# Kernel tuning notes

Hardware: AMD Instinct MI355X
Metric: run time of the kernel (lower is better)

## Reference

```python
import jax, jax.numpy as jnp
import numpy as np

# dims
T, B, D = 128, 512, 512          # seq, batch, d_input = dim_aug_state*n_agent
M, H, DH, DFF = 6, 2, 32, 64     # mem_len, heads, d_head_inner, d_ff_inner
ACT = 64                          # dim_action*n_agent
BG = 0.1                          # GRU-gate bias (GTrXL)


def _ln(t, g, b):
    mu = t.mean(-1, keepdims=True)
    var = ((t - mu) ** 2).mean(-1, keepdims=True)
    return (t - mu) / jnp.sqrt(var + 1e-5) * g + b


def _rel_shift(x):
    # x: [T, J, B, H] -> TransformerXL relative shift
    Tq, J = x.shape[0], x.shape[1]
    zp = jnp.zeros((Tq, 1) + x.shape[2:], x.dtype)
    x = jnp.concatenate([zp, x], axis=1)              # [T, J+1, B, H]
    x = x.reshape((J + 1, Tq) + x.shape[2:])[1:]      # [J, T, B, H]
    return x.reshape((Tq, J) + x.shape[2:])


def _gate(x, y, W, b):
    # GRU-style gating g(x, y): x = residual stream, y = new branch output
    lin = lambda t, i: t @ W[i] + b[i]
    r = jax.nn.sigmoid(lin(y, 0) + lin(x, 1))
    z = jax.nn.sigmoid(lin(y, 2) + lin(x, 3) - BG)
    h = jnp.tanh(lin(y, 4) + (r * x) @ W[5] + b[5])
    return (1.0 - z) * x + z * h


def setup_inputs() -> dict:
    key = jax.random.key(0)
    ks = iter(jax.random.split(key, 32))
    rn = lambda shape, s=0.02: jax.random.normal(next(ks), shape, jnp.float32) * s
    return dict(
        aug_states=jax.random.normal(next(ks), (T, B, D), jnp.float32),
        action=jax.random.normal(next(ks), (B, ACT), jnp.float32),
        memory=jnp.zeros((M, B, D), jnp.float32),
        W_q=rn((D, H * DH)), W_kv=rn((D, 2 * H * DH)), W_p=rn((D, H * DH)), W_out=rn((H * DH, D)),
        u=rn((H, DH)), v=rn((H, DH)),
        ln1_g=jnp.ones(D), ln1_b=jnp.zeros(D), ln2_g=jnp.ones(D), ln2_b=jnp.zeros(D),
        ff_W1=rn((D, DFF)), ff_b1=jnp.zeros(DFF), ff_W2=rn((DFF, D)), ff_b2=jnp.zeros(D),
        g1_W=rn((6, D, D)), g1_b=jnp.zeros((6, D)), g2_W=rn((6, D, D)), g2_b=jnp.zeros((6, D)),
        d1_W=rn((D, 1024)), d1_b=jnp.zeros(1024),
        d2_W=rn((1024 + ACT, 512)), d2_b=jnp.zeros(512),
        d3_W=rn((512, 300)), d3_b=jnp.zeros(300),
        d4_W=rn((300, 1)), d4_b=jnp.zeros(1),
    )


def reference(aug_states, action, memory, W_q, W_kv, W_p, W_out, u, v,
              ln1_g, ln1_b, ln2_g, ln2_b, ff_W1, ff_b1, ff_W2, ff_b2,
              g1_W, g1_b, g2_W, g2_b, d1_W, d1_b, d2_W, d2_b, d3_W, d3_b, d4_W, d4_b):
    x = aug_states                                    # [T, B, D]
    J = T + M
    # sinusoidal relative position embeddings for positions J-1 .. 0
    pos = jnp.arange(J - 1, -1, -1.0, dtype=jnp.float32)
    inv_freq = 1.0 / (10000.0 ** (jnp.arange(0, D, 2, dtype=jnp.float32) / D))
    si = pos[:, None] * inv_freq[None, :]
    pos_emb = jnp.concatenate([jnp.sin(si), jnp.cos(si)], axis=-1)   # [J, D]

    # --- stable (pre-LN + gated) TransformerXL layer ---
    src2 = _ln(x, ln1_g, ln1_b)
    cat = jnp.concatenate([memory, src2], axis=0)     # [J, B, D]
    k, vv = jnp.split(cat @ W_kv, 2, axis=-1)
    q = (src2 @ W_q).reshape(T, B, H, DH)
    k = k.reshape(J, B, H, DH)
    vv = vv.reshape(J, B, H, DH)
    p = (pos_emb @ W_p).reshape(J, H, DH)
    content = jnp.einsum("ibhd,jbhd->ijbh", q + u, k)
    position = _rel_shift(jnp.einsum("ibhd,jhd->ijbh", q + v, p))
    attn = content + position                         # [T, J, B, H]
    mask = jnp.arange(J)[None, :] > (jnp.arange(T)[:, None] + M)     # causal w/ memory offset
    attn = jnp.where(mask[:, :, None, None], -jnp.inf, attn)
    attn = jax.nn.softmax(attn * (1.0 / np.sqrt(DH)), axis=1)
    av = jnp.einsum("ijbh,jbhd->ibhd", attn, vv).reshape(T, B, H * DH)
    src = _gate(x, av @ W_out, g1_W, g1_b)
    ff = jax.nn.relu(_ln(src, ln2_g, ln2_b) @ ff_W1 + ff_b1) @ ff_W2 + ff_b2
    out = _gate(src, ff, g2_W, g2_b)                  # [T, B, D]

    # --- mean pool + MLP critic head ---
    ts = out.mean(axis=0)                             # [B, D]
    h1 = jax.nn.relu(ts @ d1_W + d1_b)
    h = jnp.concatenate([h1, action], axis=1)
    h = jax.nn.relu(h @ d2_W + d2_b)
    h = jax.nn.relu(h @ d3_W + d3_b)
    return jax.nn.relu(h @ d4_W + d4_b)               # [B, 1]
```

## Files before the change

### kernel.cpp

```cpp
#include <hip/hip_runtime.h>
#include <math.h>

namespace {

constexpr int kT = 128, kB = 512, kD = 512, kM = 6, kH = 2;
constexpr int kJ = kT + kM;
constexpr float kBG = 0.1f;
constexpr int kTB = kT * kB;
constexpr int kBK = 32;

typedef __attribute__((ext_vector_type(8))) short bf16x8;
typedef __attribute__((ext_vector_type(4))) float f32x4;
typedef __attribute__((ext_vector_type(8))) unsigned short us8;
typedef __attribute__((ext_vector_type(4))) unsigned short us4;

__device__ __forceinline__ float sigmoidf_(float x) {
  return 1.0f / (1.0f + __expf(-x));
}

__device__ __forceinline__ unsigned short bf16u(float f) {
  union { float f; unsigned u; } c; c.f = f;
  unsigned r = c.u + 0x7fffu + ((c.u >> 16) & 1u);
  return (unsigned short)(r >> 16);
}

__device__ __forceinline__ float b2f(unsigned short u) {
  union { unsigned u; float f; } c; c.u = (unsigned)u << 16;
  return c.f;
}

__device__ __forceinline__ void gl_lds16(const void* g, void* l) {
  __builtin_amdgcn_global_load_lds(
      (const __attribute__((address_space(1))) unsigned int*)g,
      (__attribute__((address_space(3))) unsigned int*)l, 16, 0, 0);
}

template <int N>
__device__ __forceinline__ void wvm_() {
  asm volatile("s_waitcnt vmcnt(%0)" :: "n"(N) : "memory");
}
__device__ __forceinline__ void bar_() { __builtin_amdgcn_s_barrier(); }
__device__ __forceinline__ void cfence_() { asm volatile("" ::: "memory"); }


__global__ __launch_bounds__(256) void transp_kernel(const float* __restrict__ W,
                                                     unsigned short* __restrict__ Wt,
                                                     int K, int N) {
  __shared__ float t[32][33];
  const int n0 = blockIdx.x * 32, k0 = blockIdx.y * 32;
  const float* Wb = W + (size_t)blockIdx.z * K * N;
  unsigned short* Wtb = Wt + (size_t)blockIdx.z * K * N;
  int tx = threadIdx.x & 31, ty = threadIdx.x >> 5;
#pragma unroll
  for (int r = 0; r < 32; r += 8)
    t[ty + r][tx] = Wb[(size_t)(k0 + ty + r) * N + n0 + tx];
  __syncthreads();
#pragma unroll
  for (int r = 0; r < 32; r += 8)
    Wtb[(size_t)(n0 + ty + r) * K + k0 + tx] = bf16u(t[tx][ty + r]);
}

__global__ __launch_bounds__(256) void conv_bf16_kernel(const float* __restrict__ in,
                                                        unsigned short* __restrict__ outb,
                                                        size_t n) {
  size_t idx = ((size_t)blockIdx.x * 256 + threadIdx.x) * 8;
  if (idx >= n) return;
  float4 a = *(const float4*)(in + idx);
  float4 c = *(const float4*)(in + idx + 4);
  us8 o;
  o[0] = bf16u(a.x); o[1] = bf16u(a.y); o[2] = bf16u(a.z); o[3] = bf16u(a.w);
  o[4] = bf16u(c.x); o[5] = bf16u(c.y); o[6] = bf16u(c.z); o[7] = bf16u(c.w);
  *(us8*)(outb + idx) = o;
}

__global__ __launch_bounds__(256) void ln1_dual_kernel(const float* __restrict__ in,
                                                       const float* __restrict__ g,
                                                       const float* __restrict__ b,
                                                       unsigned short* __restrict__ outLN,
                                                       unsigned short* __restrict__ outRaw,
                                                       int nrows) {
  int wave = threadIdx.x >> 6, lane = threadIdx.x & 63;
  int row = blockIdx.x * 4 + wave;
  if (row >= nrows) return;
  const float* p = in + (size_t)row * kD + lane * 8;
  float4 a = *(const float4*)p;
  float4 c = *(const float4*)(p + 4);
  float v[8] = {a.x, a.y, a.z, a.w, c.x, c.y, c.z, c.w};
  float s = 0.f;
#pragma unroll
  for (int i = 0; i < 8; ++i) s += v[i];
#pragma unroll
  for (int off = 32; off; off >>= 1) s += __shfl_xor(s, off);
  float mu = s * (1.0f / 512.0f);
  float q = 0.f;
#pragma unroll
  for (int i = 0; i < 8; ++i) { float d = v[i] - mu; q += d * d; }
#pragma unroll
  for (int off = 32; off; off >>= 1) q += __shfl_xor(q, off);
  float rstd = rsqrtf(q * (1.0f / 512.0f) + 1e-5f);
  us8 oln, oraw;
#pragma unroll
  for (int i = 0; i < 8; ++i) {
    int col = lane * 8 + i;
    oln[i] = bf16u((v[i] - mu) * rstd * g[col] + b[col]);
    oraw[i] = bf16u(v[i]);
  }
  size_t off8 = (size_t)row * kD + lane * 8;
  *(us8*)(outLN + off8) = oln;
  *(us8*)(outRaw + off8) = oraw;
}

__global__ __launch_bounds__(256) void ln_b16_kernel(const unsigned short* __restrict__ in,
                                                     const float* __restrict__ g,
                                                     const float* __restrict__ b,
                                                     unsigned short* __restrict__ outb,
                                                     int nrows) {
  int wave = threadIdx.x >> 6, lane = threadIdx.x & 63;
  int row = blockIdx.x * 4 + wave;
  if (row >= nrows) return;
  us8 iv = *(const us8*)(in + (size_t)row * kD + lane * 8);
  float v[8];
#pragma unroll
  for (int i = 0; i < 8; ++i) v[i] = b2f(iv[i]);
  float s = 0.f;
#pragma unroll
  for (int i = 0; i < 8; ++i) s += v[i];
#pragma unroll
  for (int off = 32; off; off >>= 1) s += __shfl_xor(s, off);
  float mu = s * (1.0f / 512.0f);
  float q = 0.f;
#pragma unroll
  for (int i = 0; i < 8; ++i) { float d = v[i] - mu; q += d * d; }
#pragma unroll
  for (int off = 32; off; off >>= 1) q += __shfl_xor(q, off);
  float rstd = rsqrtf(q * (1.0f / 512.0f) + 1e-5f);
  us8 o;
#pragma unroll
  for (int i = 0; i < 8; ++i) {
    int col = lane * 8 + i;
    o[i] = bf16u((v[i] - mu) * rstd * g[col] + b[col]);
  }
  *(us8*)(outb + (size_t)row * kD + lane * 8) = o;
}

template <int TN, int EPI>
__global__ __launch_bounds__(256) void mfma_gemm_bt(
    const unsigned short* __restrict__ A, const unsigned short* __restrict__ Bt,
    int K, const float* __restrict__ bias, void* __restrict__ Cv, int N) {
  constexpr int MI = (TN == 128) ? 4 : 2;
  constexpr int NJ = 4;
  constexpr int BCH = TN * 64 / 1024;
  constexpr int NLD = 2 + BCH / 4;
  __shared__ __align__(16) unsigned short As[3][128 * kBK];
  __shared__ __align__(16) unsigned short Bs[3][TN * kBK];
  const int tid = threadIdx.x;
  const int lane = tid & 63, wv = tid >> 6;
  const int ml = lane & 15, qd = lane >> 4;
  const int swc = ((lane & 3) ^ ((lane >> 3) & 3)) * 16;
  const int qdx = qd ^ ((ml >> 1) & 3);
  const int m0 = blockIdx.y * 128, n0 = blockIdx.x * TN;
  const int mw0 = (TN == 128) ? (wv >> 1) * 64 : wv * 32;
  const int nw0 = (TN == 128) ? (wv & 1) * 64 : 0;
  const size_t ldA = (size_t)K * 2, ldB = (size_t)K * 2;
  const char* Ab = (const char*)A + (size_t)m0 * ldA;
  const char* Bb = (const char*)Bt + (size_t)n0 * ldB;
  auto stg = [&](int k0, int buf) {
#pragma unroll
    for (int c = wv; c < 8; c += 4) {
      int fb = c * 1024 + lane * 16;
      gl_lds16(Ab + (size_t)(fb >> 6) * ldA + swc + (size_t)k0 * 2,
               (char*)As[buf] + c * 1024 + lane * 16);
    }
#pragma unroll
    for (int c = wv; c < BCH; c += 4) {
      int fb = c * 1024 + lane * 16;
      gl_lds16(Bb + (size_t)(fb >> 6) * ldB + swc + (size_t)k0 * 2,
               (char*)Bs[buf] + c * 1024 + lane * 16);
    }
  };
  f32x4 acc[MI][NJ];
#pragma unroll
  for (int i = 0; i < MI; ++i)
#pragma unroll
    for (int j = 0; j < NJ; ++j) acc[i][j] = (f32x4)0.f;
  stg(0, 0);
  stg(kBK, 1);
  int cb = 0;
  for (int k0 = 0; k0 < K; k0 += kBK) {
    const int sb = (cb == 0) ? 2 : cb - 1;
    if (k0 + 2 * kBK < K) { stg(k0 + 2 * kBK, sb); wvm_<2 * NLD>(); }
    else if (k0 + kBK < K) { wvm_<NLD>(); }
    else { wvm_<0>(); }
    bar_(); cfence_();
    bf16x8 af[MI], bfr[NJ];
#pragma unroll
    for (int i = 0; i < MI; ++i)
      af[i] = *(const bf16x8*)(As[cb] + (mw0 + i * 16 + ml) * kBK + qdx * 8);
#pragma unroll
    for (int j = 0; j < NJ; ++j)
      bfr[j] = *(const bf16x8*)(Bs[cb] + (nw0 + j * 16 + ml) * kBK + qdx * 8);
#pragma unroll
    for (int i = 0; i < MI; ++i)
#pragma unroll
      for (int j = 0; j < NJ; ++j)
        acc[i][j] = __builtin_amdgcn_mfma_f32_16x16x32_bf16(af[i], bfr[j], acc[i][j], 0, 0, 0);
    cfence_(); bar_();
    cb = (cb == 2) ? 0 : cb + 1;
  }
#pragma unroll
  for (int i = 0; i < MI; ++i)
#pragma unroll
    for (int j = 0; j < NJ; ++j)
#pragma unroll
      for (int r = 0; r < 4; ++r) {
        int m = m0 + mw0 + i * 16 + qd * 4 + r;
        int n = n0 + nw0 + j * 16 + ml;
        float val = acc[i][j][r];
        if (EPI >= 2) val += bias[n];
        if (EPI == 2) val = fmaxf(val, 0.f);
        size_t idx = (size_t)m * N + n;
        if (EPI == 0) ((float*)Cv)[idx] = val;
        else ((unsigned short*)Cv)[idx] = bf16u(val);
      }
}

template <int NBLOG>
__device__ __forceinline__ void xcd_decode(int& m0, int& n0, int tileN) {
  const int L = blockIdx.x;
  const int xcd = L & 7;
  const int s = L >> 3;
  const int mgPerX = (int)(gridDim.x >> (3 + NBLOG));
  const int mg = xcd * mgPerX + (s >> NBLOG);
  const int nb = s & ((1 << NBLOG) - 1);
  m0 = mg * 128;
  n0 = nb * tileN;
}

__global__ __launch_bounds__(512, 4) void mfma_gate_rz(
    const unsigned short* __restrict__ Yb, const unsigned short* __restrict__ Xb,
    const unsigned short* __restrict__ Wt, const float* __restrict__ gb,
    unsigned short* __restrict__ RX, unsigned short* __restrict__ Zq) {
  __shared__ __align__(16) unsigned short As[3][128 * kBK];
  __shared__ __align__(16) unsigned short Bs[3][256 * kBK];
  const int tid = threadIdx.x;
  const int lane = tid & 63, wv = tid >> 6;
  const int ml = lane & 15, qd = lane >> 4;
  const int swc = ((lane & 3) ^ ((lane >> 3) & 3)) * 16;
  const int qdx = qd ^ ((ml >> 1) & 3);
  int m0, n0;
  xcd_decode<2>(m0, n0, 256);
  const int nhalf = n0 >> 9;
  const int n0e = n0 & 511;
  const int mw0 = (wv & 1) * 64, nw0 = (wv >> 1) * 64;
  const size_t ld = (size_t)kD * 2;
  const size_t DD = (size_t)kD * kD;
  const char* Abp[2], *Bbp[2];
  {
    const unsigned short* Ap[2] = {Yb, Xb};
#pragma unroll
    for (int p = 0; p < 2; ++p) {
      Abp[p] = (const char*)Ap[p] + (size_t)m0 * ld;
      Bbp[p] = (const char*)(Wt + (size_t)(2 * nhalf + p) * DD) + (size_t)n0e * ld;
    }
  }
  auto stg = [&](const char* Ab, const char* Bb, int k0, int buf) {
    {
      int fb = wv * 1024 + lane * 16;
      gl_lds16(Ab + (size_t)(fb >> 6) * ld + swc + (size_t)k0 * 2,
               (char*)As[buf] + fb);
    }
#pragma unroll
    for (int c = wv; c < 16; c += 8) {
      int fb = c * 1024 + lane * 16;
      gl_lds16(Bb + (size_t)(fb >> 6) * ld + swc + (size_t)k0 * 2,
               (char*)Bs[buf] + fb);
    }
  };
  f32x4 acc[4][4];
#pragma unroll
  for (int i = 0; i < 4; ++i)
#pragma unroll
    for (int j = 0; j < 4; ++j) acc[i][j] = (f32x4)0.f;
  stg(Abp[0], Bbp[0], 0, 0);
  stg(Abp[0], Bbp[0], kBK, 1);
  int cb = 0;
#pragma unroll
  for (int p = 0; p < 2; ++p) {
    for (int k = 0; k < 16; ++k) {
      const int sb = (cb == 0) ? 2 : cb - 1;
      if (k < 14) { stg(Abp[p], Bbp[p], (k + 2) * kBK, sb); wvm_<6>(); }
      else if (p < 1) { stg(Abp[p + 1], Bbp[p + 1], (k - 14) * kBK, sb); wvm_<6>(); }
      else if (k == 14) { wvm_<3>(); }
      else { wvm_<0>(); }
      bar_(); cfence_();
      bf16x8 af[4], bfr[4];
#pragma unroll
      for (int i = 0; i < 4; ++i)
        af[i] = *(const bf16x8*)(As[cb] + (mw0 + i * 16 + ml) * kBK + qdx * 8);
#pragma unroll
      for (int j = 0; j < 4; ++j)
        bfr[j] = *(const bf16x8*)(Bs[cb] + (nw0 + j * 16 + ml) * kBK + qdx * 8);
#pragma unroll
      for (int i = 0; i < 4; ++i)
#pragma unroll
        for (int j = 0; j < 4; ++j)
          acc[i][j] = __builtin_amdgcn_mfma_f32_16x16x32_bf16(af[i], bfr[j], acc[i][j], 0, 0, 0);
      cfence_(); bar_();
      cb = (cb == 2) ? 0 : cb + 1;
    }
  }
  if (nhalf == 0) {
#pragma unroll
    for (int i = 0; i < 4; ++i)
#pragma unroll
      for (int j = 0; j < 4; ++j)
#pragma unroll
        for (int r = 0; r < 4; ++r) {
          int m = m0 + mw0 + i * 16 + qd * 4 + r;
          int n = n0e + nw0 + j * 16 + ml;
          float rg = sigmoidf_(acc[i][j][r] + gb[n] + gb[kD + n]);
          size_t idx = (size_t)m * kD + n;
          RX[idx] = bf16u(rg * b2f(Xb[idx]));
        }
  } else {
#pragma unroll
    for (int i = 0; i < 4; ++i)
#pragma unroll
      for (int j = 0; j < 4; ++j)
#pragma unroll
        for (int r = 0; r < 4; ++r) {
          int m = m0 + mw0 + i * 16 + qd * 4 + r;
          int n = n0e + nw0 + j * 16 + ml;
          float z = sigmoidf_(acc[i][j][r] + gb[2 * kD + n] + gb[3 * kD + n] - kBG);
          Zq[(size_t)m * kD + n] = (unsigned short)(z * 65535.f + 0.5f);
        }
  }
}

template <bool POOL>
__global__ __launch_bounds__(512, 4) void mfma_gate_h(
    const unsigned short* __restrict__ Yb, const unsigned short* __restrict__ RXb,
    const unsigned short* __restrict__ Xb, const unsigned short* __restrict__ Wt,
    const float* __restrict__ gb, const unsigned short* __restrict__ Zq,
    unsigned short* __restrict__ OUTb, float* __restrict__ TS, int rowoff) {
  __shared__ __align__(16) unsigned short As[3][128 * kBK];
  __shared__ __align__(16) unsigned short Bs[3][256 * kBK];
  const int tid = threadIdx.x;
  const int lane = tid & 63, wv = tid >> 6;
  const int ml = lane & 15, qd = lane >> 4;
  const int swc = ((lane & 3) ^ ((lane >> 3) & 3)) * 16;
  const int qdx = qd ^ ((ml >> 1) & 3);
  int m0, n0;
  xcd_decode<1>(m0, n0, 256);
  const int mw0 = (wv & 1) * 64, nw0 = (wv >> 1) * 64;
  const size_t ld = (size_t)kD * 2;
  const size_t DD = (size_t)kD * kD;
  const char* Abp[2], *Bbp[2];
  {
    const unsigned short* Ap[2] = {Yb, RXb};
#pragma unroll
    for (int p = 0; p < 2; ++p) {
      Abp[p] = (const char*)Ap[p] + (size_t)m0 * ld;
      Bbp[p] = (const char*)(Wt + (size_t)(4 + p) * DD) + (size_t)n0 * ld;
    }
  }
  auto stg = [&](const char* Ab, const char* Bb, int k0, int buf) {
    {
      int fb = wv * 1024 + lane * 16;
      gl_lds16(Ab + (size_t)(fb >> 6) * ld + swc + (size_t)k0 * 2,
               (char*)As[buf] + fb);
    }
#pragma unroll
    for (int c = wv; c < 16; c += 8) {
      int fb = c * 1024 + lane * 16;
      gl_lds16(Bb + (size_t)(fb >> 6) * ld + swc + (size_t)k0 * 2,
               (char*)Bs[buf] + fb);
    }
  };
  f32x4 acc[4][4];
#pragma unroll
  for (int i = 0; i < 4; ++i)
#pragma unroll
    for (int j = 0; j < 4; ++j) acc[i][j] = (f32x4)0.f;
  stg(Abp[0], Bbp[0], 0, 0);
  stg(Abp[0], Bbp[0], kBK, 1);
  int cb = 0;
#pragma unroll
  for (int p = 0; p < 2; ++p) {
    for (int k = 0; k < 16; ++k) {
      const int sb = (cb == 0) ? 2 : cb - 1;
      if (k < 14) { stg(Abp[p], Bbp[p], (k + 2) * kBK, sb); wvm_<6>(); }
      else if (p < 1) { stg(Abp[p + 1], Bbp[p + 1], (k - 14) * kBK, sb); wvm_<6>(); }
      else if (k == 14) { wvm_<3>(); }
      else { wvm_<0>(); }
      bar_(); cfence_();
      bf16x8 af[4], bfr[4];
#pragma unroll
      for (int i = 0; i < 4; ++i)
        af[i] = *(const bf16x8*)(As[cb] + (mw0 + i * 16 + ml) * kBK + qdx * 8);
#pragma unroll
      for (int j = 0; j < 4; ++j)
        bfr[j] = *(const bf16x8*)(Bs[cb] + (nw0 + j * 16 + ml) * kBK + qdx * 8);
#pragma unroll
      for (int i = 0; i < 4; ++i)
#pragma unroll
        for (int j = 0; j < 4; ++j)
          acc[i][j] = __builtin_amdgcn_mfma_f32_16x16x32_bf16(af[i], bfr[j], acc[i][j], 0, 0, 0);
      cfence_(); bar_();
      cb = (cb == 2) ? 0 : cb + 1;
    }
  }
#pragma unroll
  for (int i = 0; i < 4; ++i)
#pragma unroll
    for (int j = 0; j < 4; ++j)
#pragma unroll
      for (int r = 0; r < 4; ++r) {
        int m = m0 + mw0 + i * 16 + qd * 4 + r;
        int n = n0 + nw0 + j * 16 + ml;
        size_t idx = (size_t)m * kD + n;
        float z = (float)Zq[idx] * (1.0f / 65535.0f);
        float hc = tanhf(acc[i][j][r] + gb[4 * kD + n] + gb[5 * kD + n]);
        float val = (1.0f - z) * b2f(Xb[idx]) + z * hc;
        if (POOL) {
          int b = (rowoff + m) & (kB - 1);
          atomicAdd(TS + (size_t)b * kD + n, val * (1.0f / kT));
        } else {
          OUTb[idx] = bf16u(val);
        }
      }
}

__global__ __launch_bounds__(64) void posp_kernel(const float* __restrict__ Wp,
                                                  float* __restrict__ P) {
  __shared__ float emb[512];
  int jj = blockIdx.x;
  int t = threadIdx.x;
  float pos = (float)(kJ - 1 - jj);
#pragma unroll
  for (int r = 0; r < 8; ++r) {
    int d = t + r * 64;
    int i = (d < 256) ? d : d - 256;
    float invf = expf(-((float)(2 * i) * (1.0f / 512.0f)) * 9.210340371976184f);
    float si = pos * invf;
    emb[d] = (d < 256) ? sinf(si) : cosf(si);
  }
  __syncthreads();
  float acc = 0.f;
  for (int d = 0; d < 512; ++d) acc = fmaf(emb[d], Wp[d * 64 + t], acc);
  P[jj * 64 + t] = acc;
}

__global__ __launch_bounds__(128) void attn_kernel(
    const float* __restrict__ Q, const unsigned short* __restrict__ KV,
    const float* __restrict__ P, const float* __restrict__ U,
    const float* __restrict__ V, unsigned short* __restrict__ AV) {
  __shared__ float ks[kJ][32];
  __shared__ float vs[kJ][32];
  __shared__ float ps[32][kJ + 2];
  const int b = blockIdx.x, h = blockIdx.y;
  const int tid = threadIdx.x;
  for (int idx = tid; idx < kJ * 8; idx += 128) {
    int j = idx >> 3, seg = idx & 7;
    const unsigned short* src = KV + ((size_t)(j * kB + b)) * 128 + h * 32 + seg * 4;
    us4 kq = *(const us4*)src;
    us4 vq = *(const us4*)(src + 64);
#pragma unroll
    for (int e = 0; e < 4; ++e) {
      ks[j][seg * 4 + e] = b2f(kq[e]);
      vs[j][seg * 4 + e] = b2f(vq[e]);
    }
  }
  for (int idx = tid; idx < kJ * 8; idx += 128) {
    int j = idx >> 3, seg = idx & 7;
    float4 pq = *(const float4*)(P + j * 64 + h * 32 + seg * 4);
    ps[seg * 4 + 0][j] = pq.x;
    ps[seg * 4 + 1][j] = pq.y;
    ps[seg * 4 + 2][j] = pq.z;
    ps[seg * 4 + 3][j] = pq.w;
  }
  __syncthreads();
  const int i = tid;
  float qu[32], qv[32];
  const float* qp = Q + ((size_t)(i * kB + b)) * 64 + h * 32;
#pragma unroll
  for (int d = 0; d < 32; ++d) {
    float qd = qp[d];
    qu[d] = qd + U[h * 32 + d];
    qv[d] = qd + V[h * 32 + d];
  }
  float m = -INFINITY, l = 0.f, acc[32] = {};
  const float scale = 0.17677669529663687f;
  for (int j = 0; j <= i + kM; ++j) {
    float s = 0.f;
#pragma unroll
    for (int d = 0; d < 32; d += 4) {
      float4 k4 = *(const float4*)&ks[j][d];
      s = fmaf(qu[d + 0], k4.x, s);
      s = fmaf(qu[d + 1], k4.y, s);
      s = fmaf(qu[d + 2], k4.z, s);
      s = fmaf(qu[d + 3], k4.w, s);
    }
    int jj = j + (kT - 1) - i;
#pragma unroll
    for (int d = 0; d < 32; ++d) s = fmaf(qv[d], ps[d][jj], s);
    float ls = s * scale;
    float nm = fmaxf(m, ls);
    float w = __expf(ls - nm);
    float f = __expf(m - nm);
    l = l * f + w;
#pragma unroll
    for (int d = 0; d < 32; d += 4) {
      float4 v4 = *(const float4*)&vs[j][d];
      acc[d + 0] = fmaf(acc[d + 0], f, w * v4.x);
      acc[d + 1] = fmaf(acc[d + 1], f, w * v4.y);
      acc[d + 2] = fmaf(acc[d + 2], f, w * v4.z);
      acc[d + 3] = fmaf(acc[d + 3], f, w * v4.w);
    }
    m = nm;
  }
  float inv = 1.0f / l;
  unsigned short* o = AV + ((size_t)(i * kB + b)) * 64 + h * 32;
#pragma unroll
  for (int d = 0; d < 32; ++d) o[d] = bf16u(acc[d] * inv);
}

template <int ACTF, bool DUAL>
__global__ __launch_bounds__(256) void gemm_kernel(
    const float* __restrict__ A1, const float* __restrict__ Bm1, int K1,
    const float* __restrict__ A2, const float* __restrict__ Bm2, int K2,
    const float* __restrict__ bias, float* __restrict__ C, int Mrows, int N) {
  __shared__ float As[16][68];
  __shared__ float Bs[16][68];
  const int tid = threadIdx.x;
  const int tx = tid & 15, ty = tid >> 4;
  const int m0 = blockIdx.y * 64, n0 = blockIdx.x * 64;
  const int ar = tid >> 2, aseg = tid & 3;
  float acc[4][4] = {};
#pragma unroll
  for (int pass = 0; pass < (DUAL ? 2 : 1); ++pass) {
    const float* A = (DUAL && pass) ? A2 : A1;
    const float* Bm = (DUAL && pass) ? Bm2 : Bm1;
    const int K = (DUAL && pass) ? K2 : K1;
    for (int k0 = 0; k0 < K; k0 += 16) {
      {
        int row = m0 + ar;
        int kb = k0 + aseg * 4;
        float x0 = 0.f, x1 = 0.f, x2 = 0.f, x3 = 0.f;
        if (row < Mrows) {
          const float* ap = A + (size_t)row * K + kb;
          if (kb + 3 < K) {
            float4 t = *(const float4*)ap;
            x0 = t.x; x1 = t.y; x2 = t.z; x3 = t.w;
          } else {
            if (kb + 0 < K) x0 = ap[0];
            if (kb + 1 < K) x1 = ap[1];
            if (kb + 2 < K) x2 = ap[2];
          }
        }
        As[aseg * 4 + 0][ar] = x0;
        As[aseg * 4 + 1][ar] = x1;
        As[aseg * 4 + 2][ar] = x2;
        As[aseg * 4 + 3][ar] = x3;
      }
      {
        int krow = k0 + ty;
        int nb = n0 + tx * 4;
        float y0 = 0.f, y1 = 0.f, y2 = 0.f, y3 = 0.f;
        if (krow < K) {
          const float* bp = Bm + (size_t)krow * N + nb;
          if (nb + 3 < N) {
            float4 t = *(const float4*)bp;
            y0 = t.x; y1 = t.y; y2 = t.z; y3 = t.w;
          } else {
            if (nb + 0 < N) y0 = bp[0];
            if (nb + 1 < N) y1 = bp[1];
            if (nb + 2 < N) y2 = bp[2];
          }
        }
        *(float4*)&Bs[ty][tx * 4] = make_float4(y0, y1, y2, y3);
      }
      __syncthreads();
#pragma unroll
      for (int kk = 0; kk < 16; ++kk) {
        float a[4], bb[4];
        *(float4*)a = *(const float4*)&As[kk][ty * 4];
        *(float4*)bb = *(const float4*)&Bs[kk][tx * 4];
#pragma unroll
        for (int i = 0; i < 4; ++i)
#pragma unroll
          for (int j = 0; j < 4; ++j) acc[i][j] = fmaf(a[i], bb[j], acc[i][j]);
      }
      __syncthreads();
    }
  }
#pragma unroll
  for (int i = 0; i < 4; ++i) {
    int m = m0 + ty * 4 + i;
    if (m >= Mrows) continue;
#pragma unroll
    for (int j = 0; j < 4; ++j) {
      int n = n0 + tx * 4 + j;
      if (n >= N) continue;
      float val = acc[i][j];
      if (bias) val += bias[n];
      if (ACTF == 1) val = fmaxf(val, 0.f);
      C[(size_t)m * N + n] = val;
    }
  }
}

}

extern "C" void kernel_launch(void* const* d_in, const int* in_sizes, int n_in,
                              void* d_out, int out_size, void* d_ws, size_t ws_size,
                              hipStream_t stream) {
  (void)in_sizes; (void)n_in; (void)out_size;
  const float* aug    = (const float*)d_in[0];
  const float* action = (const float*)d_in[1];
  const float* memory = (const float*)d_in[2];
  const float* W_q    = (const float*)d_in[3];
  const float* W_kv   = (const float*)d_in[4];
  const float* W_p    = (const float*)d_in[5];
  const float* W_out  = (const float*)d_in[6];
  const float* u      = (const float*)d_in[7];
  const float* v      = (const float*)d_in[8];
  const float* ln1_g  = (const float*)d_in[9];
  const float* ln1_b  = (const float*)d_in[10];
  const float* ln2_g  = (const float*)d_in[11];
  const float* ln2_b  = (const float*)d_in[12];
  const float* ff_W1  = (const float*)d_in[13];
  const float* ff_b1  = (const float*)d_in[14];
  const float* ff_W2  = (const float*)d_in[15];
  const float* ff_b2  = (const float*)d_in[16];
  const float* g1_W   = (const float*)d_in[17];
  const float* g1_b   = (const float*)d_in[18];
  const float* g2_W   = (const float*)d_in[19];
  const float* g2_b   = (const float*)d_in[20];
  const float* d1_W   = (const float*)d_in[21];
  const float* d1_b   = (const float*)d_in[22];
  const float* d2_W   = (const float*)d_in[23];
  const float* d2_b   = (const float*)d_in[24];
  const float* d3_W   = (const float*)d_in[25];
  const float* d3_b   = (const float*)d_in[26];
  const float* d4_W   = (const float*)d_in[27];
  const float* d4_b   = (const float*)d_in[28];
  float* out = (float*)d_out;

  char* base = (char*)d_ws;
  auto alloc = [&](size_t bytes) -> char* {
    char* p = base;
    base += (bytes + 255) & ~(size_t)255;
    return p;
  };
  unsigned short* Wqt  = (unsigned short*)alloc((size_t)64 * 512 * 2);
  unsigned short* Wkvt = (unsigned short*)alloc((size_t)128 * 512 * 2);
  unsigned short* Wot  = (unsigned short*)alloc((size_t)512 * 64 * 2);
  unsigned short* Wf1t = (unsigned short*)alloc((size_t)64 * 512 * 2);
  unsigned short* Wf2t = (unsigned short*)alloc((size_t)512 * 64 * 2);
  unsigned short* G1t  = (unsigned short*)alloc((size_t)6 * 512 * 512 * 2);
  unsigned short* G2t  = (unsigned short*)alloc((size_t)6 * 512 * 512 * 2);
  unsigned short* Memb = (unsigned short*)alloc((size_t)3072 * 512 * 2);
  unsigned short* KVb  = (unsigned short*)alloc((size_t)kJ * kB * 128 * 2);
  float* Qb  = (float*)alloc((size_t)kTB * 64 * 4);
  unsigned short* AVb = (unsigned short*)alloc((size_t)kTB * 64 * 2);
  unsigned short* Xb  = (unsigned short*)alloc((size_t)kTB * kD * 2);
  float* Pb  = (float*)alloc((size_t)kJ * 64 * 4);
  float* TSb = (float*)alloc((size_t)kB * kD * 4);
  float* H1b = (float*)alloc((size_t)kB * 1024 * 4);
  float* H2b = (float*)alloc((size_t)kB * 512 * 4);
  float* H3b = (float*)alloc((size_t)kB * 320 * 4);
  size_t fixedBytes = (size_t)(base - (char*)d_ws);
  const size_t ln1Bytes = (size_t)kTB * kD * 2;
  int nch = 1;
  while (nch < 32) {
    size_t chunkBytes = (size_t)(kTB / nch) * 4224 + 4096;
    size_t reuse = chunkBytes > ln1Bytes ? chunkBytes : ln1Bytes;
    if (fixedBytes + reuse <= ws_size) break;
    nch <<= 1;
  }
  const int CR = kTB / nch;
  char* R = base;
  unsigned short* L1b = (unsigned short*)R;
  char* rp = R;
  auto ralloc = [&](size_t bytes) -> char* {
    char* p = rp;
    rp += (bytes + 255) & ~(size_t)255;
    return p;
  };
  unsigned short* Ycb   = (unsigned short*)ralloc((size_t)CR * 512 * 2);
  unsigned short* RXcb  = (unsigned short*)ralloc((size_t)CR * 512 * 2);
  unsigned short* SRCcb = (unsigned short*)ralloc((size_t)CR * 512 * 2);
  unsigned short* LN2cb = (unsigned short*)ralloc((size_t)CR * 512 * 2);
  unsigned short* F1cb  = (unsigned short*)ralloc((size_t)CR * 64 * 2);
  unsigned short* Zqb = LN2cb;

  const float* np = nullptr;
  const int MG = CR / 128;

  hipMemsetAsync(TSb, 0, (size_t)kB * kD * sizeof(float), stream);
  transp_kernel<<<dim3(2, 16, 1), 256, 0, stream>>>(W_q, Wqt, 512, 64);
  transp_kernel<<<dim3(4, 16, 1), 256, 0, stream>>>(W_kv, Wkvt, 512, 128);
  transp_kernel<<<dim3(16, 2, 1), 256, 0, stream>>>(W_out, Wot, 64, 512);
  transp_kernel<<<dim3(2, 16, 1), 256, 0, stream>>>(ff_W1, Wf1t, 512, 64);
  transp_kernel<<<dim3(16, 2, 1), 256, 0, stream>>>(ff_W2, Wf2t, 64, 512);
  transp_kernel<<<dim3(16, 16, 6), 256, 0, stream>>>(g1_W, G1t, 512, 512);
  transp_kernel<<<dim3(16, 16, 6), 256, 0, stream>>>(g2_W, G2t, 512, 512);
  conv_bf16_kernel<<<(3072 * 512 / 8 + 255) / 256, 256, 0, stream>>>(
      memory, Memb, (size_t)3072 * 512);
  ln1_dual_kernel<<<kTB / 4, 256, 0, stream>>>(aug, ln1_g, ln1_b, L1b, Xb, kTB);
  mfma_gemm_bt<128, 1><<<dim3(1, 3072 / 128), 256, 0, stream>>>(
      Memb, Wkvt, 512, np, KVb, 128);
  mfma_gemm_bt<128, 1><<<dim3(1, kTB / 128), 256, 0, stream>>>(
      L1b, Wkvt, 512, np, KVb + (size_t)3072 * 128, 128);
  mfma_gemm_bt<64, 0><<<dim3(1, kTB / 128), 256, 0, stream>>>(
      L1b, Wqt, 512, np, Qb, 64);
  posp_kernel<<<kJ, 64, 0, stream>>>(W_p, Pb);
  attn_kernel<<<dim3(kB, kH), 128, 0, stream>>>(Qb, KVb, Pb, u, v, AVb);

  for (int c = 0; c < nch; ++c) {
    const int R0 = c * CR;
    const unsigned short* Xc = Xb + (size_t)R0 * kD;
    mfma_gemm_bt<128, 1><<<dim3(4, MG), 256, 0, stream>>>(
        AVb + (size_t)R0 * 64, Wot, 64, np, Ycb, 512);
    mfma_gate_rz<<<4 * MG, 512, 0, stream>>>(Ycb, Xc, G1t, g1_b, RXcb, Zqb);
    mfma_gate_h<false><<<2 * MG, 512, 0, stream>>>(
        Ycb, RXcb, Xc, G1t, g1_b, Zqb, SRCcb, nullptr, R0);
    ln_b16_kernel<<<CR / 4, 256, 0, stream>>>(SRCcb, ln2_g, ln2_b, LN2cb, CR);
    mfma_gemm_bt<64, 2><<<dim3(1, MG), 256, 0, stream>>>(
        LN2cb, Wf1t, 512, ff_b1, F1cb, 64);
    mfma_gemm_bt<128, 3><<<dim3(4, MG), 256, 0, stream>>>(
        F1cb, Wf2t, 64, ff_b2, Ycb, 512);
    mfma_gate_rz<<<4 * MG, 512, 0, stream>>>(Ycb, SRCcb, G2t, g2_b, RXcb, Zqb);
    mfma_gate_h<true><<<2 * MG, 512, 0, stream>>>(
        Ycb, RXcb, SRCcb, G2t, g2_b, Zqb, nullptr, TSb, R0);
  }

  gemm_kernel<1, false><<<dim3(16, kB / 64), 256, 0, stream>>>(
      TSb, d1_W, 512, np, np, 0, d1_b, H1b, kB, 1024);
  gemm_kernel<1, true><<<dim3(8, kB / 64), 256, 0, stream>>>(
      H1b, d2_W, 1024, action, d2_W + (size_t)1024 * 512, 64, d2_b, H2b, kB, 512);
  gemm_kernel<1, false><<<dim3(5, kB / 64), 256, 0, stream>>>(
      H2b, d3_W, 512, np, np, 0, d3_b, H3b, kB, 300);
  gemm_kernel<1, false><<<dim3(1, kB / 64), 256, 0, stream>>>(
      H3b, d4_W, 300, np, np, 0, d4_b, out, kB, 1);
}
```

Measured before the change: 1.524 ms.

## Shrink gate GEMM tiles to 128x128, drop LDS swizzle, add MFMA priority

The gate GEMM kernels go from 512-thread blocks with 128x256 tiles to 256-thread blocks with 128x128 tiles, doubling grid size and halving LDS per block. The XOR swizzle on LDS staging and fragment reads is removed from all MFMA GEMMs, so addresses become linear. s_setprio is raised around the MFMA inner loops. The aim is more resident blocks and simpler addressing, at the risk of LDS bank conflicts and less B-tile reuse per block.

```diff
diff --git a/kernel.cpp b/kernel.cpp
--- a/kernel.cpp
+++ b/kernel.cpp
@@ -41,7 +41,6 @@
 }
 __device__ __forceinline__ void bar_() { __builtin_amdgcn_s_barrier(); }
 __device__ __forceinline__ void cfence_() { asm volatile("" ::: "memory"); }
-
 
 __global__ __launch_bounds__(256) void transp_kernel(const float* __restrict__ W,
                                                      unsigned short* __restrict__ Wt,
@@ -156,8 +155,6 @@
   const int tid = threadIdx.x;
   const int lane = tid & 63, wv = tid >> 6;
   const int ml = lane & 15, qd = lane >> 4;
-  const int swc = ((lane & 3) ^ ((lane >> 3) & 3)) * 16;
-  const int qdx = qd ^ ((ml >> 1) & 3);
   const int m0 = blockIdx.y * 128, n0 = blockIdx.x * TN;
   const int mw0 = (TN == 128) ? (wv >> 1) * 64 : wv * 32;
   const int nw0 = (TN == 128) ? (wv & 1) * 64 : 0;
@@ -168,14 +165,14 @@
 #pragma unroll
     for (int c = wv; c < 8; c += 4) {
       int fb = c * 1024 + lane * 16;
-      gl_lds16(Ab + (size_t)(fb >> 6) * ldA + swc + (size_t)k0 * 2,
-               (char*)As[buf] + c * 1024 + lane * 16);
+      gl_lds16(Ab + (size_t)(fb >> 6) * ldA + (fb & 63) + (size_t)k0 * 2,
+               (char*)As[buf] + fb);
     }
 #pragma unroll
     for (int c = wv; c < BCH; c += 4) {
       int fb = c * 1024 + lane * 16;
-      gl_lds16(Bb + (size_t)(fb >> 6) * ldB + swc + (size_t)k0 * 2,
-               (char*)Bs[buf] + c * 1024 + lane * 16);
+      gl_lds16(Bb + (size_t)(fb >> 6) * ldB + (fb & 63) + (size_t)k0 * 2,
+               (char*)Bs[buf] + fb);
     }
   };
   f32x4 acc[MI][NJ];
@@ -195,15 +192,17 @@
     bf16x8 af[MI], bfr[NJ];
 #pragma unroll
     for (int i = 0; i < MI; ++i)
-      af[i] = *(const bf16x8*)(As[cb] + (mw0 + i * 16 + ml) * kBK + qdx * 8);
+      af[i] = *(const bf16x8*)(As[cb] + (mw0 + i * 16 + ml) * kBK + qd * 8);
 #pragma unroll
     for (int j = 0; j < NJ; ++j)
-      bfr[j] = *(const bf16x8*)(Bs[cb] + (nw0 + j * 16 + ml) * kBK + qdx * 8);
+      bfr[j] = *(const bf16x8*)(Bs[cb] + (nw0 + j * 16 + ml) * kBK + qd * 8);
+    __builtin_amdgcn_s_setprio(1);
 #pragma unroll
     for (int i = 0; i < MI; ++i)
 #pragma unroll
       for (int j = 0; j < NJ; ++j)
         acc[i][j] = __builtin_amdgcn_mfma_f32_16x16x32_bf16(af[i], bfr[j], acc[i][j], 0, 0, 0);
+    __builtin_amdgcn_s_setprio(0);
     cfence_(); bar_();
     cb = (cb == 2) ? 0 : cb + 1;
   }
@@ -236,25 +235,23 @@
   n0 = nb * tileN;
 }
 
-__global__ __launch_bounds__(512, 4) void mfma_gate_rz(
+__global__ __launch_bounds__(256) void mfma_gate_rz(
     const unsigned short* __restrict__ Yb, const unsigned short* __restrict__ Xb,
     const unsigned short* __restrict__ Wt, const float* __restrict__ gb,
     unsigned short* __restrict__ RX, unsigned short* __restrict__ Zq) {
   __shared__ __align__(16) unsigned short As[3][128 * kBK];
-  __shared__ __align__(16) unsigned short Bs[3][256 * kBK];
+  __shared__ __align__(16) unsigned short Bs[3][128 * kBK];
   const int tid = threadIdx.x;
   const int lane = tid & 63, wv = tid >> 6;
   const int ml = lane & 15, qd = lane >> 4;
-  const int swc = ((lane & 3) ^ ((lane >> 3) & 3)) * 16;
-  const int qdx = qd ^ ((ml >> 1) & 3);
   int m0, n0;
-  xcd_decode<2>(m0, n0, 256);
+  xcd_decode<3>(m0, n0, 128);
   const int nhalf = n0 >> 9;
   const int n0e = n0 & 511;
-  const int mw0 = (wv & 1) * 64, nw0 = (wv >> 1) * 64;
+  const int mw0 = (wv >> 1) * 64, nw0 = (wv & 1) * 64;
   const size_t ld = (size_t)kD * 2;
   const size_t DD = (size_t)kD * kD;
-  const char* Abp[2], *Bbp[2];
+  const char* Abp[2]; const char* Bbp[2];
   {
     const unsigned short* Ap[2] = {Yb, Xb};
 #pragma unroll
@@ -264,16 +261,12 @@
     }
   }
   auto stg = [&](const char* Ab, const char* Bb, int k0, int buf) {
-    {
-      int fb = wv * 1024 + lane * 16;
-      gl_lds16(Ab + (size_t)(fb >> 6) * ld + swc + (size_t)k0 * 2,
-               (char*)As[buf] + fb);
-    }
-#pragma unroll
-    for (int c = wv; c < 16; c += 8) {
+#pragma unroll
+    for (int c = wv; c < 8; c += 4) {
       int fb = c * 1024 + lane * 16;
-      gl_lds16(Bb + (size_t)(fb >> 6) * ld + swc + (size_t)k0 * 2,
-               (char*)Bs[buf] + fb);
+      size_t go = (size_t)(fb >> 6) * ld + (fb & 63) + (size_t)k0 * 2;
+      gl_lds16(Ab + go, (char*)As[buf] + fb);
+      gl_lds16(Bb + go, (char*)Bs[buf] + fb);
     }
   };
   f32x4 acc[4][4];
@@ -288,23 +281,25 @@
   for (int p = 0; p < 2; ++p) {
     for (int k = 0; k < 16; ++k) {
       const int sb = (cb == 0) ? 2 : cb - 1;
-      if (k < 14) { stg(Abp[p], Bbp[p], (k + 2) * kBK, sb); wvm_<6>(); }
-      else if (p < 1) { stg(Abp[p + 1], Bbp[p + 1], (k - 14) * kBK, sb); wvm_<6>(); }
-      else if (k == 14) { wvm_<3>(); }
+      if (k < 14) { stg(Abp[p], Bbp[p], (k + 2) * kBK, sb); wvm_<8>(); }
+      else if (p < 1) { stg(Abp[p + 1], Bbp[p + 1], (k - 14) * kBK, sb); wvm_<8>(); }
+      else if (k == 14) { wvm_<4>(); }
       else { wvm_<0>(); }
       bar_(); cfence_();
       bf16x8 af[4], bfr[4];
 #pragma unroll
       for (int i = 0; i < 4; ++i)
-        af[i] = *(const bf16x8*)(As[cb] + (mw0 + i * 16 + ml) * kBK + qdx * 8);
+        af[i] = *(const bf16x8*)(As[cb] + (mw0 + i * 16 + ml) * kBK + qd * 8);
 #pragma unroll
       for (int j = 0; j < 4; ++j)
-        bfr[j] = *(const bf16x8*)(Bs[cb] + (nw0 + j * 16 + ml) * kBK + qdx * 8);
+        bfr[j] = *(const bf16x8*)(Bs[cb] + (nw0 + j * 16 + ml) * kBK + qd * 8);
+      __builtin_amdgcn_s_setprio(1);
 #pragma unroll
       for (int i = 0; i < 4; ++i)
 #pragma unroll
         for (int j = 0; j < 4; ++j)
           acc[i][j] = __builtin_amdgcn_mfma_f32_16x16x32_bf16(af[i], bfr[j], acc[i][j], 0, 0, 0);
+      __builtin_amdgcn_s_setprio(0);
       cfence_(); bar_();
       cb = (cb == 2) ? 0 : cb + 1;
     }
@@ -338,24 +333,22 @@
 }
 
 template <bool POOL>
-__global__ __launch_bounds__(512, 4) void mfma_gate_h(
+__global__ __launch_bounds__(256) void mfma_gate_h(
     const unsigned short* __restrict__ Yb, const unsigned short* __restrict__ RXb,
     const unsigned short* __restrict__ Xb, const unsigned short* __restrict__ Wt,
     const float* __restrict__ gb, const unsigned short* __restrict__ Zq,
     unsigned short* __restrict__ OUTb, float* __restrict__ TS, int rowoff) {
   __shared__ __align__(16) unsigned short As[3][128 * kBK];
-  __shared__ __align__(16) unsigned short Bs[3][256 * kBK];
+  __shared__ __align__(16) unsigned short Bs[3][128 * kBK];
   const int tid = threadIdx.x;
   const int lane = tid & 63, wv = tid >> 6;
   const int ml = lane & 15, qd = lane >> 4;
-  const int swc = ((lane & 3) ^ ((lane >> 3) & 3)) * 16;
-  const int qdx = qd ^ ((ml >> 1) & 3);
   int m0, n0;
-  xcd_decode<1>(m0, n0, 256);
-  const int mw0 = (wv & 1) * 64, nw0 = (wv >> 1) * 64;
+  xcd_decode<2>(m0, n0, 128);
+  const int mw0 = (wv >> 1) * 64, nw0 = (wv & 1) * 64;
   const size_t ld = (size_t)kD * 2;
   const size_t DD = (size_t)kD * kD;
-  const char* Abp[2], *Bbp[2];
+  const char* Abp[2]; const char* Bbp[2];
   {
     const unsigned short* Ap[2] = {Yb, RXb};
 #pragma unroll
@@ -365,16 +358,12 @@
     }
   }
   auto stg = [&](const char* Ab, const char* Bb, int k0, int buf) {
-    {
-      int fb = wv * 1024 + lane * 16;
-      gl_lds16(Ab + (size_t)(fb >> 6) * ld + swc + (size_t)k0 * 2,
-               (char*)As[buf] + fb);
-    }
-#pragma unroll
-    for (int c = wv; c < 16; c += 8) {
+#pragma unroll
+    for (int c = wv; c < 8; c += 4) {
       int fb = c * 1024 + lane * 16;
-      gl_lds16(Bb + (size_t)(fb >> 6) * ld + swc + (size_t)k0 * 2,
-               (char*)Bs[buf] + fb);
+      size_t go = (size_t)(fb >> 6) * ld + (fb & 63) + (size_t)k0 * 2;
+      gl_lds16(Ab + go, (char*)As[buf] + fb);
+      gl_lds16(Bb + go, (char*)Bs[buf] + fb);
     }
   };
   f32x4 acc[4][4];
@@ -389,23 +378,25 @@
   for (int p = 0; p < 2; ++p) {
     for (int k = 0; k < 16; ++k) {
       const int sb = (cb == 0) ? 2 : cb - 1;
-      if (k < 14) { stg(Abp[p], Bbp[p], (k + 2) * kBK, sb); wvm_<6>(); }
-      else if (p < 1) { stg(Abp[p + 1], Bbp[p + 1], (k - 14) * kBK, sb); wvm_<6>(); }
-      else if (k == 14) { wvm_<3>(); }
+      if (k < 14) { stg(Abp[p], Bbp[p], (k + 2) * kBK, sb); wvm_<8>(); }
+      else if (p < 1) { stg(Abp[p + 1], Bbp[p + 1], (k - 14) * kBK, sb); wvm_<8>(); }
+      else if (k == 14) { wvm_<4>(); }
       else { wvm_<0>(); }
       bar_(); cfence_();
       bf16x8 af[4], bfr[4];
 #pragma unroll
       for (int i = 0; i < 4; ++i)
-        af[i] = *(const bf16x8*)(As[cb] + (mw0 + i * 16 + ml) * kBK + qdx * 8);
+        af[i] = *(const bf16x8*)(As[cb] + (mw0 + i * 16 + ml) * kBK + qd * 8);
 #pragma unroll
       for (int j = 0; j < 4; ++j)
-        bfr[j] = *(const bf16x8*)(Bs[cb] + (nw0 + j * 16 + ml) * kBK + qdx * 8);
+        bfr[j] = *(const bf16x8*)(Bs[cb] + (nw0 + j * 16 + ml) * kBK + qd * 8);
+      __builtin_amdgcn_s_setprio(1);
 #pragma unroll
       for (int i = 0; i < 4; ++i)
 #pragma unroll
         for (int j = 0; j < 4; ++j)
           acc[i][j] = __builtin_amdgcn_mfma_f32_16x16x32_bf16(af[i], bfr[j], acc[i][j], 0, 0, 0);
+      __builtin_amdgcn_s_setprio(0);
       cfence_(); bar_();
       cb = (cb == 2) ? 0 : cb + 1;
     }
@@ -723,16 +714,16 @@
     const unsigned short* Xc = Xb + (size_t)R0 * kD;
     mfma_gemm_bt<128, 1><<<dim3(4, MG), 256, 0, stream>>>(
         AVb + (size_t)R0 * 64, Wot, 64, np, Ycb, 512);
-    mfma_gate_rz<<<4 * MG, 512, 0, stream>>>(Ycb, Xc, G1t, g1_b, RXcb, Zqb);
-    mfma_gate_h<false><<<2 * MG, 512, 0, stream>>>(
+    mfma_gate_rz<<<8 * MG, 256, 0, stream>>>(Ycb, Xc, G1t, g1_b, RXcb, Zqb);
+    mfma_gate_h<false><<<4 * MG, 256, 0, stream>>>(
         Ycb, RXcb, Xc, G1t, g1_b, Zqb, SRCcb, nullptr, R0);
     ln_b16_kernel<<<CR / 4, 256, 0, stream>>>(SRCcb, ln2_g, ln2_b, LN2cb, CR);
     mfma_gemm_bt<64, 2><<<dim3(1, MG), 256, 0, stream>>>(
         LN2cb, Wf1t, 512, ff_b1, F1cb, 64);
     mfma_gemm_bt<128, 3><<<dim3(4, MG), 256, 0, stream>>>(
         F1cb, Wf2t, 64, ff_b2, Ycb, 512);
-    mfma_gate_rz<<<4 * MG, 512, 0, stream>>>(Ycb, SRCcb, G2t, g2_b, RXcb, Zqb);
-    mfma_gate_h<true><<<2 * MG, 512, 0, stream>>>(
+    mfma_gate_rz<<<8 * MG, 256, 0, stream>>>(Ycb, SRCcb, G2t, g2_b, RXcb, Zqb);
+    mfma_gate_h<true><<<4 * MG, 256, 0, stream>>>(
         Ycb, RXcb, SRCcb, G2t, g2_b, Zqb, nullptr, TSb, R0);
   }
 
```

New measurement: 1.547 ms. About the same (+1.5%).
